# Performance work log

Measured on AMD Instinct MI355X. Metric: run time of the kernel, lower is better.

The kernel has to match this reference:

```python
import jax, jax.numpy as jnp
import numpy as np

PARTS = (0.0, 0.25, 0.5, 0.75, 1.0)
N = 16777216


def setup_inputs() -> dict:
    key = jax.random.key(0)
    kx, ky, kd = jax.random.split(key, 3)
    x = jax.random.normal(kx, (N, 2), dtype=jnp.float32)
    y = jax.random.normal(ky, (N, 2), dtype=jnp.float32)
    dist = jax.random.uniform(kd, (N,), dtype=jnp.float32)
    return {"x": x, "y": y, "dist": dist}


def _complex_abs(v):
    # fastmri.complex_abs: sqrt(re^2 + im^2) over last dim of size 2
    return jnp.sqrt(jnp.sum(v * v, axis=-1))


def reference(x, y, dist):
    # Per-element squared errors computed once, then masked-reduced per radial bin.
    diff2_sum = jnp.sum((x - y) ** 2, axis=-1)        # [N] sum over the 2 components
    abs_diff2 = (_complex_abs(x) - _complex_abs(y)) ** 2  # [N]

    loss = jnp.float32(0.0)
    for i in range(len(PARTS) - 1):
        r0, r1 = PARTS[i], PARTS[i + 1]
        mask = (dist >= r0) & (dist <= r1)            # inclusive both ends, as in torch code
        cnt = jnp.sum(mask)                           # number of selected points
        # mse over x[ind] of shape [cnt, 2] -> divide by 2*cnt elements
        mse = jnp.sum(jnp.where(mask, diff2_sum, 0.0)) / jnp.maximum(2 * cnt, 1)
        mse_abs = jnp.sum(jnp.where(mask, abs_diff2, 0.0)) / jnp.maximum(cnt, 1)
        loss = loss + jnp.where(cnt > 0, mse + 0.1 * mse_abs, 0.0)
    return loss
```

## Files before the change

kernel.cpp:

```cpp
#include <hip/hip_runtime.h>

#define NBINS 4
#define BLOCK 256
#define WAVES_PER_BLOCK (BLOCK / 64)
#define NBLOCKS 1024

struct WS {
    float sum_d2[NBINS];
    float sum_ad2[NBINS];
    unsigned int cnt[NBINS];
};

__device__ __forceinline__ void accum_point(float x0, float x1, float y0, float y1,
                                            float d,
                                            float (&s_d2)[NBINS], float (&s_ad2)[NBINS],
                                            unsigned int (&s_cnt)[NBINS]) {
    float dx0 = x0 - y0, dx1 = x1 - y1;
    float d2 = dx0 * dx0 + dx1 * dx1;
    float ax = sqrtf(x0 * x0 + x1 * x1);
    float ay = sqrtf(y0 * y0 + y1 * y1);
    float da = ax - ay;
    float ad2 = da * da;
    const float bounds[NBINS + 1] = {0.0f, 0.25f, 0.5f, 0.75f, 1.0f};
#pragma unroll
    for (int b = 0; b < NBINS; ++b) {
        if (d >= bounds[b] && d <= bounds[b + 1]) {
            s_d2[b] += d2;
            s_ad2[b] += ad2;
            s_cnt[b] += 1u;
        }
    }
}

__global__ __launch_bounds__(BLOCK) void radial_loss_main(
    const float* __restrict__ x, const float* __restrict__ y,
    const float* __restrict__ dist, WS* __restrict__ ws, int n) {
    float s_d2[NBINS] = {0.f, 0.f, 0.f, 0.f};
    float s_ad2[NBINS] = {0.f, 0.f, 0.f, 0.f};
    unsigned int s_cnt[NBINS] = {0u, 0u, 0u, 0u};

    const int tid = blockIdx.x * blockDim.x + threadIdx.x;
    const int stride = gridDim.x * blockDim.x;
    const int n4 = n >> 2;

    const float4* __restrict__ x4 = (const float4*)x;
    const float4* __restrict__ y4 = (const float4*)y;
    const float4* __restrict__ d4 = (const float4*)dist;

    for (int i = tid; i < n4; i += stride) {
        float4 xa = x4[2 * i];
        float4 xb = x4[2 * i + 1];
        float4 ya = y4[2 * i];
        float4 yb = y4[2 * i + 1];
        float4 dd = d4[i];
        accum_point(xa.x, xa.y, ya.x, ya.y, dd.x, s_d2, s_ad2, s_cnt);
        accum_point(xa.z, xa.w, ya.z, ya.w, dd.y, s_d2, s_ad2, s_cnt);
        accum_point(xb.x, xb.y, yb.x, yb.y, dd.z, s_d2, s_ad2, s_cnt);
        accum_point(xb.z, xb.w, yb.z, yb.w, dd.w, s_d2, s_ad2, s_cnt);
    }
    for (int i = (n4 << 2) + tid; i < n; i += stride) {
        accum_point(x[2 * i], x[2 * i + 1], y[2 * i], y[2 * i + 1], dist[i],
                    s_d2, s_ad2, s_cnt);
    }

#pragma unroll
    for (int off = 32; off > 0; off >>= 1) {
#pragma unroll
        for (int b = 0; b < NBINS; ++b) {
            s_d2[b] += __shfl_down(s_d2[b], off);
            s_ad2[b] += __shfl_down(s_ad2[b], off);
            s_cnt[b] += __shfl_down(s_cnt[b], off);
        }
    }

    __shared__ float sm_d2[WAVES_PER_BLOCK][NBINS];
    __shared__ float sm_ad2[WAVES_PER_BLOCK][NBINS];
    __shared__ unsigned int sm_cnt[WAVES_PER_BLOCK][NBINS];
    const int wave = threadIdx.x >> 6;
    const int lane = threadIdx.x & 63;
    if (lane == 0) {
#pragma unroll
        for (int b = 0; b < NBINS; ++b) {
            sm_d2[wave][b] = s_d2[b];
            sm_ad2[wave][b] = s_ad2[b];
            sm_cnt[wave][b] = s_cnt[b];
        }
    }
    __syncthreads();
    if (threadIdx.x < NBINS) {
        const int b = threadIdx.x;
        float td2 = 0.f, tad2 = 0.f;
        unsigned int tc = 0u;
#pragma unroll
        for (int w = 0; w < WAVES_PER_BLOCK; ++w) {
            td2 += sm_d2[w][b];
            tad2 += sm_ad2[w][b];
            tc += sm_cnt[w][b];
        }
        atomicAdd(&ws->sum_d2[b], td2);
        atomicAdd(&ws->sum_ad2[b], tad2);
        atomicAdd(&ws->cnt[b], tc);
    }
}

__global__ void radial_loss_final(const WS* __restrict__ ws, float* __restrict__ out) {
    if (threadIdx.x == 0 && blockIdx.x == 0) {
        float loss = 0.f;
#pragma unroll
        for (int b = 0; b < NBINS; ++b) {
            unsigned int c = ws->cnt[b];
            if (c > 0u) {
                float fc = (float)c;
                loss += ws->sum_d2[b] / (2.0f * fc) + 0.1f * (ws->sum_ad2[b] / fc);
            }
        }
        out[0] = loss;
    }
}

extern "C" void kernel_launch(void* const* d_in, const int* in_sizes, int n_in,
                              void* d_out, int out_size, void* d_ws, size_t ws_size,
                              hipStream_t stream) {
    const float* x = (const float*)d_in[0];
    const float* y = (const float*)d_in[1];
    const float* dist = (const float*)d_in[2];
    float* out = (float*)d_out;
    WS* ws = (WS*)d_ws;
    const int n = in_sizes[2];

    hipMemsetAsync(ws, 0, sizeof(WS), stream);
    radial_loss_main<<<NBLOCKS, BLOCK, 0, stream>>>(x, y, dist, ws, n);
    radial_loss_final<<<1, 64, 0, stream>>>(ws, out);
}
```

Before: 332.8 us.

## Use contiguous per-block chunks with unrolled batched loads and more blocks

Replaces the grid-stride loop with contiguous per-block chunks. Each thread now issues four float4 x, four float4 y and four float2 dist loads before computing, which raises memory-level parallelism and gives fully coalesced 16-byte accesses. The grid grows from 1024 to 2048 blocks, and block 0 handles the odd-element tail. The cost is more registers per thread and twice as many blocks doing atomic adds.

```diff
diff --git a/kernel.cpp b/kernel.cpp
--- a/kernel.cpp
+++ b/kernel.cpp
@@ -2,8 +2,9 @@
 
 #define NBINS 4
 #define BLOCK 256
+#define UNROLL 4
 #define WAVES_PER_BLOCK (BLOCK / 64)
-#define NBLOCKS 1024
+#define NBLOCKS 2048
 
 struct WS {
     float sum_d2[NBINS];
@@ -39,28 +40,43 @@
     float s_ad2[NBINS] = {0.f, 0.f, 0.f, 0.f};
     unsigned int s_cnt[NBINS] = {0u, 0u, 0u, 0u};
 
-    const int tid = blockIdx.x * blockDim.x + threadIdx.x;
-    const int stride = gridDim.x * blockDim.x;
-    const int n4 = n >> 2;
-
+    const int n2 = n >> 1;
     const float4* __restrict__ x4 = (const float4*)x;
     const float4* __restrict__ y4 = (const float4*)y;
-    const float4* __restrict__ d4 = (const float4*)dist;
+    const float2* __restrict__ dd2 = (const float2*)dist;
 
-    for (int i = tid; i < n4; i += stride) {
-        float4 xa = x4[2 * i];
-        float4 xb = x4[2 * i + 1];
-        float4 ya = y4[2 * i];
-        float4 yb = y4[2 * i + 1];
-        float4 dd = d4[i];
-        accum_point(xa.x, xa.y, ya.x, ya.y, dd.x, s_d2, s_ad2, s_cnt);
-        accum_point(xa.z, xa.w, ya.z, ya.w, dd.y, s_d2, s_ad2, s_cnt);
-        accum_point(xb.x, xb.y, yb.x, yb.y, dd.z, s_d2, s_ad2, s_cnt);
-        accum_point(xb.z, xb.w, yb.z, yb.w, dd.w, s_d2, s_ad2, s_cnt);
+    const int chunk = (n2 + NBLOCKS - 1) / NBLOCKS;
+    const int start = blockIdx.x * chunk;
+    const int end = min(start + chunk, n2);
+
+    int i = start + threadIdx.x;
+    for (; i + (UNROLL - 1) * BLOCK < end; i += UNROLL * BLOCK) {
+        float4 xv[UNROLL], yv[UNROLL];
+        float2 dv[UNROLL];
+#pragma unroll
+        for (int u = 0; u < UNROLL; ++u) xv[u] = x4[i + u * BLOCK];
+#pragma unroll
+        for (int u = 0; u < UNROLL; ++u) yv[u] = y4[i + u * BLOCK];
+#pragma unroll
+        for (int u = 0; u < UNROLL; ++u) dv[u] = dd2[i + u * BLOCK];
+#pragma unroll
+        for (int u = 0; u < UNROLL; ++u) {
+            accum_point(xv[u].x, xv[u].y, yv[u].x, yv[u].y, dv[u].x, s_d2, s_ad2, s_cnt);
+            accum_point(xv[u].z, xv[u].w, yv[u].z, yv[u].w, dv[u].y, s_d2, s_ad2, s_cnt);
+        }
     }
-    for (int i = (n4 << 2) + tid; i < n; i += stride) {
-        accum_point(x[2 * i], x[2 * i + 1], y[2 * i], y[2 * i + 1], dist[i],
-                    s_d2, s_ad2, s_cnt);
+    for (; i < end; i += BLOCK) {
+        float4 xv = x4[i];
+        float4 yv = y4[i];
+        float2 dv = dd2[i];
+        accum_point(xv.x, xv.y, yv.x, yv.y, dv.x, s_d2, s_ad2, s_cnt);
+        accum_point(xv.z, xv.w, yv.z, yv.w, dv.y, s_d2, s_ad2, s_cnt);
+    }
+    if (blockIdx.x == 0) {
+        for (int p = (n2 << 1) + threadIdx.x; p < n; p += BLOCK) {
+            accum_point(x[2 * p], x[2 * p + 1], y[2 * p], y[2 * p + 1], dist[p],
+                        s_d2, s_ad2, s_cnt);
+        }
     }
 
 #pragma unroll
```

Measured after the change: 330.9 us. Within noise of the previous version (-0.6%).
